# Optimization experiments

Measured on AMD Instinct MI355X. Metric: run time of the kernel, lower is better.

## Reference

```python
import jax, jax.numpy as jnp
import numpy as np

INPUT_DIM = 128
OUTPUT_DIM = 256
BATCH = 4096

def setup_inputs() -> dict:
    key = jax.random.key(0)
    k_x, k_w1, k_b1, k_w2, k_b2 = jax.random.split(key, 5)
    d = INPUT_DIM
    h = 2 * OUTPUT_DIM
    x = jax.random.normal(k_x, (BATCH, d), dtype=jnp.float32)
    # Linear weights stored as [in, out]; scale ~ torch default init
    W1 = jax.random.uniform(k_w1, (d * d, h), dtype=jnp.float32, minval=-1, maxval=1) / np.sqrt(d * d)
    b1 = jax.random.uniform(k_b1, (h,), dtype=jnp.float32, minval=-1, maxval=1) / np.sqrt(d * d)
    W2 = jax.random.uniform(k_w2, (h, OUTPUT_DIM), dtype=jnp.float32, minval=-1, maxval=1) / np.sqrt(h)
    b2 = jax.random.uniform(k_b2, (OUTPUT_DIM,), dtype=jnp.float32, minval=-1, maxval=1) / np.sqrt(h)
    return {"x": x, "W1": W1, "b1": b1, "W2": W2, "b2": b2}

def reference(x, W1, b1, W2, b2):
    B, d = x.shape
    # torch bmm of the two expanded copies: tp[b,i,j] = sum_k x[b,i]*x[b,j] = d * x[b,i]*x[b,j]
    tp = jnp.asarray(d, x.dtype) * jnp.einsum('bi,bj->bij', x, x)  # [B, d, d]
    flat = tp.reshape(B, d * d)
    h = jax.nn.relu(flat @ W1 + b1)  # [B, 2*output_dim]
    return h @ W2 + b2               # [B, output_dim]
```

## Files before the change

kernel.cpp:

```cpp
#include <hip/hip_runtime.h>
#include <hip/hip_bf16.h>


typedef __attribute__((ext_vector_type(8))) short short8;
typedef __attribute__((ext_vector_type(4))) float floatx4;

__device__ __forceinline__ unsigned short f2bf(float f) {
    union { float f; unsigned int u; } v; v.f = f;
    unsigned int r = v.u + 0x7fffu + ((v.u >> 16) & 1u);
    return (unsigned short)(r >> 16);
}
__device__ __forceinline__ float bf2f(unsigned short b) {
    union { unsigned int u; float f; } v; v.u = ((unsigned int)b) << 16;
    return v.f;
}

__global__ __launch_bounds__(256) void pack_w1_kernel(
    const float* __restrict__ W1, unsigned short* __restrict__ W1Tp) {
    __shared__ float tile[64][65];
    const int k0 = blockIdx.x * 64;
    const int c0 = blockIdx.y * 64;
    const int tr = threadIdx.x >> 4;
    const int tc4 = (threadIdx.x & 15) * 4;
#pragma unroll
    for (int p = 0; p < 4; ++p) {
        int k = p * 16 + tr;
        float4 v = *(const float4*)(W1 + (long)(k0 + k) * 512 + c0 + tc4);
        tile[k][tc4 + 0] = v.x; tile[k][tc4 + 1] = v.y;
        tile[k][tc4 + 2] = v.z; tile[k][tc4 + 3] = v.w;
    }
    __syncthreads();
    const int lane = threadIdx.x & 63;
    const int w = threadIdx.x >> 6;
    const int m = lane & 15, quad = lane >> 4;
#pragma unroll
    for (int pass = 0; pass < 2; ++pass) {
        int chunk = w * 2 + pass;
        int kcL = chunk & 1, c16L = chunk >> 1;
        union { unsigned short s[8]; uint4 u; } o;
#pragma unroll
        for (int j = 0; j < 8; ++j)
            o.s[j] = f2bf(tile[kcL * 32 + quad * 8 + j][c16L * 16 + m]);
        long c16g = (c0 >> 4) + c16L;
        long kcg  = (k0 >> 5) + kcL;
        *(uint4*)(W1Tp + (c16g * 512 + kcg) * 512 + lane * 8) = o.u;
    }
}

__global__ __launch_bounds__(256) void transpose_cast_kernel(
    const float* __restrict__ in, unsigned short* __restrict__ out, int R, int C) {
    __shared__ float tile[64][65];
    const int r0 = blockIdx.x * 64, c0 = blockIdx.y * 64;
    const int tr = threadIdx.x >> 4;
    const int tc4 = (threadIdx.x & 15) * 4;
#pragma unroll
    for (int p = 0; p < 4; ++p) {
        int r = p * 16 + tr;
        float4 v = *(const float4*)(in + (long)(r0 + r) * C + c0 + tc4);
        tile[r][tc4 + 0] = v.x; tile[r][tc4 + 1] = v.y;
        tile[r][tc4 + 2] = v.z; tile[r][tc4 + 3] = v.w;
    }
    __syncthreads();
#pragma unroll
    for (int p = 0; p < 4; ++p) {
        int c = p * 16 + tr;
        union { unsigned short s[4]; uint2 u; } pk;
#pragma unroll
        for (int e = 0; e < 4; ++e) pk.s[e] = f2bf(tile[tc4 + e][c]);
        *(uint2*)(out + (long)(c0 + c) * R + r0 + tc4) = pk.u;
    }
}

__global__ __launch_bounds__(256, 4) void gemm1_kernel(
    const float* __restrict__ x,
    const unsigned short* __restrict__ W1Tp,
    unsigned short* __restrict__ Pb) {
    __shared__ float xT[128][36];
    const int tid = threadIdx.x;
    const int b0 = blockIdx.x * 128;
    const int c0 = blockIdx.y * 64;
    const int zi = blockIdx.z;
    const int i0 = zi * 32;

    for (int idx = tid; idx < 128 * 32; idx += 256) {
        int bL = idx >> 5, iL = idx & 31;
        xT[bL][iL] = x[(long)(b0 + bL) * 128 + i0 + iL];
    }
    __syncthreads();

    const int wid = tid >> 6;
    const int wm = wid >> 1, wn = wid & 1;
    const int lane = tid & 63;
    const int n16 = lane & 15, quad = lane >> 4;
    const int bBase = b0 + wn * 64;
    const int c16base = (c0 >> 4) + wm * 2;
    const int bLloc = wn * 64 + n16;

    floatx4 acc[2][4];
#pragma unroll
    for (int tm = 0; tm < 2; ++tm)
#pragma unroll
        for (int tn = 0; tn < 4; ++tn) acc[tm][tn] = (floatx4){0.f, 0.f, 0.f, 0.f};
    const floatx4 zero4 = (floatx4){0.f, 0.f, 0.f, 0.f};

#pragma unroll
    for (int jh = 0; jh < 2; ++jh) {
        short8 Xf[2][4];
#pragma unroll
        for (int ks = 0; ks < 2; ++ks)
#pragma unroll
            for (int tn = 0; tn < 4; ++tn) {
                const float* xp = x + (long)(bBase + tn * 16 + n16) * 128
                                    + jh * 64 + ks * 32 + quad * 8;
                float4 v0 = *(const float4*)xp;
                float4 v1 = *(const float4*)(xp + 4);
                short8 f;
                f[0] = (short)f2bf(v0.x); f[1] = (short)f2bf(v0.y);
                f[2] = (short)f2bf(v0.z); f[3] = (short)f2bf(v0.w);
                f[4] = (short)f2bf(v1.x); f[5] = (short)f2bf(v1.y);
                f[6] = (short)f2bf(v1.z); f[7] = (short)f2bf(v1.w);
                Xf[ks][tn] = f;
            }
        const unsigned short* aBase[2][2];
#pragma unroll
        for (int tm = 0; tm < 2; ++tm)
#pragma unroll
            for (int ks = 0; ks < 2; ++ks)
                aBase[tm][ks] = W1Tp
                    + ((long)(c16base + tm) * 512 + (long)i0 * 4 + jh * 2 + ks) * 512
                    + lane * 8;

        short8 Abuf[2][2][2];
#pragma unroll
        for (int tm = 0; tm < 2; ++tm)
#pragma unroll
            for (int ks = 0; ks < 2; ++ks) {
                Abuf[0][tm][ks] = *(const short8*)(aBase[tm][ks]);
                Abuf[1][tm][ks] = *(const short8*)(aBase[tm][ks] + 2048);
            }

#pragma unroll 4
        for (int i = 0; i < 32; ++i) {
            const int st = i & 1;
            float xi[4];
#pragma unroll
            for (int tn = 0; tn < 4; ++tn)
                xi[tn] = xT[bLloc + tn * 16][i];
#pragma unroll
            for (int tm = 0; tm < 2; ++tm)
#pragma unroll
                for (int tn = 0; tn < 4; ++tn) {
                    floatx4 t = __builtin_amdgcn_mfma_f32_16x16x32_bf16(
                        Abuf[st][tm][0], Xf[0][tn], zero4, 0, 0, 0);
                    t = __builtin_amdgcn_mfma_f32_16x16x32_bf16(
                        Abuf[st][tm][1], Xf[1][tn], t, 0, 0, 0);
                    acc[tm][tn] += xi[tn] * t;
                }
            const int pi = (i + 2) & 31;
#pragma unroll
            for (int tm = 0; tm < 2; ++tm)
#pragma unroll
                for (int ks = 0; ks < 2; ++ks)
                    Abuf[st][tm][ks] =
                        *(const short8*)(aBase[tm][ks] + (long)pi * 2048);
        }
    }

    unsigned short* pb = Pb + (long)zi * (4096L * 512);
#pragma unroll
    for (int tm = 0; tm < 2; ++tm)
#pragma unroll
        for (int tn = 0; tn < 4; ++tn) {
            int b = bBase + tn * 16 + n16;
            int cb = (c16base + tm) * 16 + quad * 4;
            union { unsigned short s[4]; uint2 u; } pk;
#pragma unroll
            for (int r = 0; r < 4; ++r) pk.s[r] = f2bf(acc[tm][tn][r]);
            *(uint2*)(pb + (long)b * 512 + cb) = pk.u;
        }
}

__global__ __launch_bounds__(256) void tail_kernel(
    const unsigned short* __restrict__ Pb,
    const float* __restrict__ b1,
    const unsigned short* __restrict__ W2T,
    const float* __restrict__ b2,
    float* __restrict__ out) {
    __shared__ unsigned short hL[16][516];
    __shared__ float b1s[512];
    const int tid = threadIdx.x;
    const int b0 = blockIdx.x * 16;
    b1s[tid] = b1[tid];
    b1s[tid + 256] = b1[tid + 256];
    __syncthreads();

    const unsigned int* Pu = (const unsigned int*)Pb;
#pragma unroll 4
    for (int idx = tid; idx < 16 * 256; idx += 256) {
        int bL = idx >> 8;
        int cu = idx & 255;
        float s0 = 0.f, s1 = 0.f;
#pragma unroll
        for (int z = 0; z < 4; ++z) {
            unsigned int u = Pu[((long)z * 4096 + b0 + bL) * 256 + cu];
            s0 += bf2f((unsigned short)(u & 0xffff));
            s1 += bf2f((unsigned short)(u >> 16));
        }
        int c = cu * 2;
        float v0 = fmaxf(fmaf(128.f, s0, b1s[c]), 0.f);
        float v1 = fmaxf(fmaf(128.f, s1, b1s[c + 1]), 0.f);
        unsigned int pk = (unsigned int)f2bf(v0) | ((unsigned int)f2bf(v1) << 16);
        *(unsigned int*)&hL[bL][c] = pk;
    }
    __syncthreads();

    const int w = tid >> 6, lane = tid & 63;
    const int n16 = lane & 15, quad = lane >> 4;
    const int o0 = w * 64;
    floatx4 acc[4];
#pragma unroll
    for (int tn = 0; tn < 4; ++tn) acc[tn] = (floatx4){0.f, 0.f, 0.f, 0.f};

#pragma unroll 4
    for (int ks = 0; ks < 16; ++ks) {
        short8 Af, Bf[4];
        {
            const unsigned short* p = &hL[n16][ks * 32 + quad * 8];
            union { uint2 u[2]; short8 s; } cvt;
            cvt.u[0] = *(const uint2*)p;
            cvt.u[1] = *(const uint2*)(p + 4);
            Af = cvt.s;
        }
#pragma unroll
        for (int tn = 0; tn < 4; ++tn)
            Bf[tn] = *(const short8*)(W2T + (long)(o0 + tn * 16 + n16) * 512
                                      + ks * 32 + quad * 8);
#pragma unroll
        for (int tn = 0; tn < 4; ++tn)
            acc[tn] = __builtin_amdgcn_mfma_f32_16x16x32_bf16(
                Af, Bf[tn], acc[tn], 0, 0, 0);
    }
#pragma unroll
    for (int tn = 0; tn < 4; ++tn) {
        float bias = b2[o0 + tn * 16 + n16];
#pragma unroll
        for (int r = 0; r < 4; ++r)
            out[(long)(b0 + quad * 4 + r) * 256
                + o0 + tn * 16 + n16] = acc[tn][r] + bias;
    }
}

extern "C" void kernel_launch(void* const* d_in, const int* in_sizes, int n_in,
                              void* d_out, int out_size, void* d_ws, size_t ws_size,
                              hipStream_t stream) {
    const float* x  = (const float*)d_in[0];
    const float* W1 = (const float*)d_in[1];
    const float* b1 = (const float*)d_in[2];
    const float* W2 = (const float*)d_in[3];
    const float* b2 = (const float*)d_in[4];
    float* out = (float*)d_out;

    char* ws = (char*)d_ws;
    unsigned short* W1Tp = (unsigned short*)(ws);
    unsigned short* W2T  = (unsigned short*)(ws + 16777216);
    unsigned short* Pb   = (unsigned short*)(ws + 16777216 + 262144);

    pack_w1_kernel<<<dim3(256, 8), 256, 0, stream>>>(W1, W1Tp);
    transpose_cast_kernel<<<dim3(8, 4), 256, 0, stream>>>(W2, W2T, 512, 256);
    gemm1_kernel<<<dim3(32, 8, 4), 256, 0, stream>>>(x, W1Tp, Pb);
    tail_kernel<<<dim3(256), 256, 0, stream>>>(Pb, b1, W2T, b2, out);
}
```

Measured before the change: 184.6 us.

## Materialize outer-product tiles in LDS and accumulate directly via MFMA

Replaces the factored approach (MFMA over W1 times x_j, then scaling by x_i and accumulating in fp32 on vector units) with one that forms x_i*x_j products in bf16 in shared memory each step and feeds them to MFMA, accumulating straight into the matrix accumulators. This removes the per-i vector FMA epilogue and the extra zero-init MFMA chain, but adds two block barriers per inner iteration, LDS writes and reads, and drops the double-buffered W1 prefetch. The warp tiling also changes from 2x4 to 4x2 tiles per wave. Rounding the product to bf16 before the MFMA also shifts the numerics slightly.

```diff
diff --git a/kernel.cpp b/kernel.cpp
--- a/kernel.cpp
+++ b/kernel.cpp
@@ -13,6 +13,12 @@
 __device__ __forceinline__ float bf2f(unsigned short b) {
     union { unsigned int u; float f; } v; v.u = ((unsigned int)b) << 16;
     return v.f;
+}
+__device__ __forceinline__ unsigned int pk2bf(float a, float b) {
+    float2 p; p.x = a; p.y = b;
+    __hip_bfloat162 h = __float22bfloat162_rn(p);
+    union { __hip_bfloat162 h; unsigned int u; } cv; cv.h = h;
+    return cv.u;
 }
 
 __global__ __launch_bounds__(256) void pack_w1_kernel(
@@ -75,7 +81,8 @@
     const float* __restrict__ x,
     const unsigned short* __restrict__ W1Tp,
     unsigned short* __restrict__ Pb) {
-    __shared__ float xT[128][36];
+    __shared__ float xiT[128][34];
+    __shared__ unsigned short Bt[128][40];
     const int tid = threadIdx.x;
     const int b0 = blockIdx.x * 128;
     const int c0 = blockIdx.y * 64;
@@ -84,95 +91,71 @@
 
     for (int idx = tid; idx < 128 * 32; idx += 256) {
         int bL = idx >> 5, iL = idx & 31;
-        xT[bL][iL] = x[(long)(b0 + bL) * 128 + i0 + iL];
+        xiT[bL][iL] = x[(long)(b0 + bL) * 128 + i0 + iL];
     }
     __syncthreads();
 
     const int wid = tid >> 6;
-    const int wm = wid >> 1, wn = wid & 1;
     const int lane = tid & 63;
     const int n16 = lane & 15, quad = lane >> 4;
-    const int bBase = b0 + wn * 64;
-    const int c16base = (c0 >> 4) + wm * 2;
-    const int bLloc = wn * 64 + n16;
-
-    floatx4 acc[2][4];
-#pragma unroll
-    for (int tm = 0; tm < 2; ++tm)
-#pragma unroll
-        for (int tn = 0; tn < 4; ++tn) acc[tm][tn] = (floatx4){0.f, 0.f, 0.f, 0.f};
-    const floatx4 zero4 = (floatx4){0.f, 0.f, 0.f, 0.f};
-
-#pragma unroll
-    for (int jh = 0; jh < 2; ++jh) {
-        short8 Xf[2][4];
-#pragma unroll
-        for (int ks = 0; ks < 2; ++ks)
-#pragma unroll
-            for (int tn = 0; tn < 4; ++tn) {
-                const float* xp = x + (long)(bBase + tn * 16 + n16) * 128
-                                    + jh * 64 + ks * 32 + quad * 8;
-                float4 v0 = *(const float4*)xp;
-                float4 v1 = *(const float4*)(xp + 4);
-                short8 f;
-                f[0] = (short)f2bf(v0.x); f[1] = (short)f2bf(v0.y);
-                f[2] = (short)f2bf(v0.z); f[3] = (short)f2bf(v0.w);
-                f[4] = (short)f2bf(v1.x); f[5] = (short)f2bf(v1.y);
-                f[6] = (short)f2bf(v1.z); f[7] = (short)f2bf(v1.w);
-                Xf[ks][tn] = f;
-            }
-        const unsigned short* aBase[2][2];
-#pragma unroll
-        for (int tm = 0; tm < 2; ++tm)
-#pragma unroll
-            for (int ks = 0; ks < 2; ++ks)
-                aBase[tm][ks] = W1Tp
-                    + ((long)(c16base + tm) * 512 + (long)i0 * 4 + jh * 2 + ks) * 512
-                    + lane * 8;
-
-        short8 Abuf[2][2][2];
-#pragma unroll
-        for (int tm = 0; tm < 2; ++tm)
-#pragma unroll
-            for (int ks = 0; ks < 2; ++ks) {
-                Abuf[0][tm][ks] = *(const short8*)(aBase[tm][ks]);
-                Abuf[1][tm][ks] = *(const short8*)(aBase[tm][ks] + 2048);
-            }
-
-#pragma unroll 4
+    const int bLp = tid & 127;
+    const int jsub = tid >> 7;
+    const int c16base = c0 >> 4;
+
+    floatx4 acc[4][2];
+#pragma unroll
+    for (int tm = 0; tm < 4; ++tm)
+#pragma unroll
+        for (int tn = 0; tn < 2; ++tn) acc[tm][tn] = (floatx4){0.f, 0.f, 0.f, 0.f};
+
+    for (int jw = 0; jw < 4; ++jw) {
+        float xj[16];
+        const float* xrow = x + (long)(b0 + bLp) * 128 + jw * 32 + jsub * 16;
+#pragma unroll
+        for (int e = 0; e < 16; ++e) xj[e] = xrow[e];
+
         for (int i = 0; i < 32; ++i) {
-            const int st = i & 1;
-            float xi[4];
-#pragma unroll
-            for (int tn = 0; tn < 4; ++tn)
-                xi[tn] = xT[bLloc + tn * 16][i];
-#pragma unroll
-            for (int tm = 0; tm < 2; ++tm)
-#pragma unroll
-                for (int tn = 0; tn < 4; ++tn) {
-                    floatx4 t = __builtin_amdgcn_mfma_f32_16x16x32_bf16(
-                        Abuf[st][tm][0], Xf[0][tn], zero4, 0, 0, 0);
-                    t = __builtin_amdgcn_mfma_f32_16x16x32_bf16(
-                        Abuf[st][tm][1], Xf[1][tn], t, 0, 0, 0);
-                    acc[tm][tn] += xi[tn] * t;
-                }
-            const int pi = (i + 2) & 31;
-#pragma unroll
-            for (int tm = 0; tm < 2; ++tm)
-#pragma unroll
-                for (int ks = 0; ks < 2; ++ks)
-                    Abuf[st][tm][ks] =
-                        *(const short8*)(aBase[tm][ks] + (long)pi * 2048);
+            const int kcg = (i0 + i) * 4 + jw;
+            short8 Af0 = *(const short8*)(W1Tp + ((long)(c16base + 0) * 512 + kcg) * 512 + lane * 8);
+            short8 Af1 = *(const short8*)(W1Tp + ((long)(c16base + 1) * 512 + kcg) * 512 + lane * 8);
+            short8 Af2 = *(const short8*)(W1Tp + ((long)(c16base + 2) * 512 + kcg) * 512 + lane * 8);
+            short8 Af3 = *(const short8*)(W1Tp + ((long)(c16base + 3) * 512 + kcg) * 512 + lane * 8);
+
+            float xi = xiT[bLp][i];
+            uint4 w0, w1;
+            w0.x = pk2bf(xi * xj[0],  xi * xj[1]);
+            w0.y = pk2bf(xi * xj[2],  xi * xj[3]);
+            w0.z = pk2bf(xi * xj[4],  xi * xj[5]);
+            w0.w = pk2bf(xi * xj[6],  xi * xj[7]);
+            w1.x = pk2bf(xi * xj[8],  xi * xj[9]);
+            w1.y = pk2bf(xi * xj[10], xi * xj[11]);
+            w1.z = pk2bf(xi * xj[12], xi * xj[13]);
+            w1.w = pk2bf(xi * xj[14], xi * xj[15]);
+            *(uint4*)&Bt[bLp][jsub * 16 + 0] = w0;
+            *(uint4*)&Bt[bLp][jsub * 16 + 8] = w1;
+            __syncthreads();
+
+            short8 Bf0 = *(const short8*)&Bt[wid * 32 + n16][quad * 8];
+            short8 Bf1 = *(const short8*)&Bt[wid * 32 + 16 + n16][quad * 8];
+            acc[0][0] = __builtin_amdgcn_mfma_f32_16x16x32_bf16(Af0, Bf0, acc[0][0], 0, 0, 0);
+            acc[0][1] = __builtin_amdgcn_mfma_f32_16x16x32_bf16(Af0, Bf1, acc[0][1], 0, 0, 0);
+            acc[1][0] = __builtin_amdgcn_mfma_f32_16x16x32_bf16(Af1, Bf0, acc[1][0], 0, 0, 0);
+            acc[1][1] = __builtin_amdgcn_mfma_f32_16x16x32_bf16(Af1, Bf1, acc[1][1], 0, 0, 0);
+            acc[2][0] = __builtin_amdgcn_mfma_f32_16x16x32_bf16(Af2, Bf0, acc[2][0], 0, 0, 0);
+            acc[2][1] = __builtin_amdgcn_mfma_f32_16x16x32_bf16(Af2, Bf1, acc[2][1], 0, 0, 0);
+            acc[3][0] = __builtin_amdgcn_mfma_f32_16x16x32_bf16(Af3, Bf0, acc[3][0], 0, 0, 0);
+            acc[3][1] = __builtin_amdgcn_mfma_f32_16x16x32_bf16(Af3, Bf1, acc[3][1], 0, 0, 0);
+            __syncthreads();
         }
     }
 
     unsigned short* pb = Pb + (long)zi * (4096L * 512);
 #pragma unroll
-    for (int tm = 0; tm < 2; ++tm)
-#pragma unroll
-        for (int tn = 0; tn < 4; ++tn) {
-            int b = bBase + tn * 16 + n16;
-            int cb = (c16base + tm) * 16 + quad * 4;
+    for (int tm = 0; tm < 4; ++tm)
+#pragma unroll
+        for (int tn = 0; tn < 2; ++tn) {
+            int b = b0 + wid * 32 + tn * 16 + n16;
+            int cb = c0 + tm * 16 + quad * 4;
             union { unsigned short s[4]; uint2 u; } pk;
 #pragma unroll
             for (int r = 0; r < 4; ++r) pk.s[r] = f2bf(acc[tm][tn][r]);
```

Result: slower. 199.9 us (+8.3%).
